# Optimization experiments

Measured on AMD Instinct MI355X. Metric: run time of the kernel, lower is better.

## Reference

```python
import jax, jax.numpy as jnp
import numpy as np

PRED_LEN = 256
K = 32
LOW_FREQ = 1


def setup_inputs() -> dict:
    key = jax.random.key(0)
    x = jax.random.normal(key, (8, 1024, 512), dtype=jnp.float32)
    return {"x": x}


def _fourier_layer(x):
    b, t, d = x.shape
    # per-channel standardization over time (torch .std is unbiased -> ddof=1)
    x_mean = jnp.mean(x, axis=1, keepdims=True)                      # (b,1,d)
    x_std = jnp.std(x, axis=1, keepdims=True, ddof=1) + 1e-8         # (b,1,d)
    xs = jnp.clip((x - x_mean) / x_std, -2.0, 2.0) + 1e-9

    # rfft over time; t is even and LOW_FREQ < t//2 -> drop DC..low_freq-1 and Nyquist
    x_freq = jnp.fft.rfft(xs, axis=1)[:, LOW_FREQ:-1]                # (b,N,d) complex64
    n_freq = x_freq.shape[1]
    f = jnp.fft.rfftfreq(t).astype(jnp.float32)[LOW_FREQ:n_freq + LOW_FREQ]  # (N,)

    # top-k frequencies by amplitude, independently per (batch, channel)
    amp_all = jnp.abs(x_freq).astype(jnp.float32)                    # (b,N,d)
    _, idx = jax.lax.top_k(jnp.transpose(amp_all, (0, 2, 1)), K)     # (b,d,k)
    idx = jnp.transpose(idx, (0, 2, 1))                              # (b,k,d)
    xf = jnp.take_along_axis(x_freq, idx, axis=1)                    # (b,k,d)
    f_sel = f[idx]                                                   # (b,k,d)

    # extrapolate: conjugate pair -> real signal, sum of k cosines
    xf2 = jnp.concatenate([xf, jnp.conj(xf)], axis=1)                # (b,2k,d)
    f2 = jnp.concatenate([f_sel, -f_sel], axis=1)[:, :, None, :]     # (b,2k,1,d)
    T = t + PRED_LEN
    t_val = jnp.arange(T, dtype=jnp.float32)[None, None, :, None]    # (1,1,T,1)
    amp = (jnp.abs(xf2) / (t + 1e-8))[:, :, None, :]                 # (b,2k,1,d)
    phase = jnp.clip(jnp.angle(xf2), -np.pi, np.pi)[:, :, None, :]   # (b,2k,1,d)
    angle = 2.0 * np.pi * f2 * t_val + phase                         # (b,2k,T,d)
    angle = angle - 2.0 * np.pi * jnp.floor(angle / (2.0 * np.pi))
    x_time = jnp.sum(amp * jnp.cos(angle), axis=1)                   # (b,T,d)

    return x_time * x_std + x_mean


def reference(x):
    return _fourier_layer(x)
```

## Files before the change

kernel.cpp:

```cpp
#include <hip/hip_runtime.h>

#define T_IN 1024
#define D_DIM 512
#define T_OUT 1280
#define NPAIR 4096

__global__ __launch_bounds__(256) void transpose_kernel(const float* __restrict__ x,
                                                        float* __restrict__ xt,
                                                        double2* __restrict__ tw) {
    __shared__ float tile[64][65];
    const int b  = blockIdx.z;
    const int t0 = blockIdx.y * 64;
    const int d0 = blockIdx.x * 64;
    const int dl = threadIdx.x & 63;
    const int r0 = threadIdx.x >> 6;

    if (blockIdx.x < 4 && blockIdx.y == 0 && blockIdx.z == 0) {
        int m = blockIdx.x * 256 + threadIdx.x;
        double th = (6.283185307179586476925286766559 / 1024.0) * (double)m;
        tw[m] = make_double2(cos(th), -sin(th));
    }

#pragma unroll
    for (int i = 0; i < 16; ++i) {
        int tl = r0 * 16 + i;
        tile[tl][dl] = x[((size_t)b * T_IN + (t0 + tl)) * D_DIM + d0 + dl];
    }
    __syncthreads();
#pragma unroll
    for (int i = 0; i < 16; ++i) {
        int dl2 = r0 * 16 + i;
        xt[((size_t)b * D_DIM + (d0 + dl2)) * T_IN + t0 + dl] = tile[dl][dl2];
    }
}

__device__ __forceinline__ double2 TW8(const double2* __restrict__ E, int m) {
    int r = m & 255;
    int q = (m >> 8) & 3;
    double c, s;
    if (r <= 128) { double2 t = E[r];       c = t.x; s = t.y; }
    else          { double2 t = E[256 - r]; c = t.y; s = t.x; }
    double C, S;
    switch (q) {
        case 0:  C = c;  S = s;  break;
        case 1:  C = -s; S = c;  break;
        case 2:  C = -c; S = -s; break;
        default: C = s;  S = -c; break;
    }
    return make_double2(C, -S);
}

__global__ __launch_bounds__(256) void dft_kernel(const float* __restrict__ xt,
                                                  const double2* __restrict__ twg,
                                                  float2* __restrict__ stats,
                                                  float4* __restrict__ sel) {
    __shared__ double2 uni[1024];
    __shared__ double2 tw_s[130];
    __shared__ double  red_s[16];
    double* xs_s = (double*)uni;

    const int tid  = threadIdx.x;
    const int pair = blockIdx.x;

    const float4 v = reinterpret_cast<const float4*>(xt + (size_t)pair * T_IN)[tid];

    if (tid < 130) {
        double2 t = twg[tid];
        tw_s[tid] = make_double2(t.x, -t.y);
    }

    double sum = (double)v.x + (double)v.y + (double)v.z + (double)v.w;
    double sq  = (double)v.x * v.x + (double)v.y * v.y +
                 (double)v.z * v.z + (double)v.w * v.w;
#pragma unroll
    for (int off = 32; off; off >>= 1) {
        sum += __shfl_down(sum, off);
        sq  += __shfl_down(sq, off);
    }
    const int wv   = tid >> 6;
    const int lane = tid & 63;
    if (lane == 0) { red_s[wv] = sum; red_s[8 + wv] = sq; }
    __syncthreads();
    double mean, stdp;
    {
        double s = red_s[0] + red_s[1] + red_s[2] + red_s[3];
        double q = red_s[8] + red_s[9] + red_s[10] + red_s[11];
        mean = s * (1.0 / 1024.0);
        double var = (q - 1024.0 * mean * mean) * (1.0 / 1023.0);
        var = var > 0.0 ? var : 0.0;
        stdp = sqrt(var) + 1e-8;
        if (tid == 0) stats[pair] = make_float2((float)mean, (float)stdp);
    }
    const double inv = 1.0 / stdp;
    {
        double z0 = ((double)v.x - mean) * inv;
        double z1 = ((double)v.y - mean) * inv;
        double z2 = ((double)v.z - mean) * inv;
        double z3 = ((double)v.w - mean) * inv;
        z0 = fmin(2.0, fmax(-2.0, z0)) + 1e-9;
        z1 = fmin(2.0, fmax(-2.0, z1)) + 1e-9;
        z2 = fmin(2.0, fmax(-2.0, z2)) + 1e-9;
        z3 = fmin(2.0, fmax(-2.0, z3)) + 1e-9;
        xs_s[tid * 4 + 0] = z0;
        xs_s[tid * 4 + 1] = z1;
        xs_s[tid * 4 + 2] = z2;
        xs_s[tid * 4 + 3] = z3;
    }
    __syncthreads();

    {
        int idx = tid;
#pragma unroll
        for (int rr = 0; rr < 2; ++rr) {
            if (idx < 480) {
                int t1p = 1 + (idx >> 5);
                int t2c = idx & 31;
                int ia = t1p * 32 + t2c;
                int ib = (32 - t1p) * 32 + t2c;
                double a = xs_s[ia], b = xs_s[ib];
                xs_s[ia] = a + b;
                xs_s[ib] = a - b;
            }
            idx += 256;
        }
    }
    __syncthreads();

    const int k1 = tid & 31;
    const int g  = tid >> 5;

    double2 R0, R1, R2, R3;
    {
        const double2 w = TW8(tw_s, k1 * 32);
        const double sgn16 = (k1 & 1) ? -1.0 : 1.0;

        double ar0 = xs_s[g]      + sgn16 * xs_s[512 + g];
        double ar1 = xs_s[g + 8]  + sgn16 * xs_s[512 + g + 8];
        double ar2 = xs_s[g + 16] + sgn16 * xs_s[512 + g + 16];
        double ar3 = xs_s[g + 24] + sgn16 * xs_s[512 + g + 24];
        double ai0 = 0, ai1 = 0, ai2 = 0, ai3 = 0;

        double c = w.x, s = w.y;
#pragma unroll 5
        for (int t1 = 1; t1 <= 15; ++t1) {
            const double* eb = &xs_s[t1 * 32];
            const double* ob = &xs_s[(32 - t1) * 32];
            ar0 = fma(eb[g], c, ar0);      ai0 = fma(ob[g], s, ai0);
            ar1 = fma(eb[g + 8], c, ar1);  ai1 = fma(ob[g + 8], s, ai1);
            ar2 = fma(eb[g + 16], c, ar2); ai2 = fma(ob[g + 16], s, ai2);
            ar3 = fma(eb[g + 24], c, ar3); ai3 = fma(ob[g + 24], s, ai3);
            double cn = c * w.x - s * w.y;
            double sn = s * w.x + c * w.y;
            c = cn; s = sn;
        }
        {
            double2 tm = TW8(tw_s, g * k1);
            R0 = make_double2(ar0 * tm.x - ai0 * tm.y, ar0 * tm.y + ai0 * tm.x);
        }
        {
            double2 tm = TW8(tw_s, (g + 8) * k1);
            R1 = make_double2(ar1 * tm.x - ai1 * tm.y, ar1 * tm.y + ai1 * tm.x);
        }
        {
            double2 tm = TW8(tw_s, (g + 16) * k1);
            R2 = make_double2(ar2 * tm.x - ai2 * tm.y, ar2 * tm.y + ai2 * tm.x);
        }
        {
            double2 tm = TW8(tw_s, (g + 24) * k1);
            R3 = make_double2(ar3 * tm.x - ai3 * tm.y, ar3 * tm.y + ai3 * tm.x);
        }
    }
    __syncthreads();

    uni[g * 32 + k1]        = R0;
    uni[(g + 8) * 32 + k1]  = R1;
    uni[(g + 16) * 32 + k1] = R2;
    uni[(g + 24) * 32 + k1] = R3;
    __syncthreads();

    double Ar = 0, Ai = 0, Br = 0, Bi = 0;
    {
        const double2 wa = TW8(tw_s, 32 * g);
        const double sg = (g & 1) ? -1.0 : 1.0;
        double ca = 1.0, sa = 0.0;
#pragma unroll
        for (int u = 0; u < 4; ++u) {
            {
                const int t2 = 4 * u + 0;
                double2 S  = uni[t2 * 32 + k1];
                double2 S2 = uni[(t2 + 16) * 32 + k1];
                double Ex = fma(sg, S2.x, S.x);
                double Ey = fma(sg, S2.y, S.y);
                double P = fma(Ex, ca, -(Ey * sa));
                double Q = fma(Ex, sa,  (Ey * ca));
                Ar += P; Ai += Q; Br += P; Bi += Q;
                double cn = fma(ca, wa.x, -(sa * wa.y));
                double sn = fma(sa, wa.x,  (ca * wa.y));
                ca = cn; sa = sn;
            }
            {
                const int t2 = 4 * u + 1;
                double2 S  = uni[t2 * 32 + k1];
                double2 S2 = uni[(t2 + 16) * 32 + k1];
                double Ex = fma(sg, S2.x, S.x);
                double Ey = fma(sg, S2.y, S.y);
                double P = fma(Ex, ca, -(Ey * sa));
                double Q = fma(Ex, sa,  (Ey * ca));
                Ar += P; Ai += Q; Br += Q; Bi -= P;
                double cn = fma(ca, wa.x, -(sa * wa.y));
                double sn = fma(sa, wa.x,  (ca * wa.y));
                ca = cn; sa = sn;
            }
            {
                const int t2 = 4 * u + 2;
                double2 S  = uni[t2 * 32 + k1];
                double2 S2 = uni[(t2 + 16) * 32 + k1];
                double Ex = fma(sg, S2.x, S.x);
                double Ey = fma(sg, S2.y, S.y);
                double P = fma(Ex, ca, -(Ey * sa));
                double Q = fma(Ex, sa,  (Ey * ca));
                Ar += P; Ai += Q; Br -= P; Bi -= Q;
                double cn = fma(ca, wa.x, -(sa * wa.y));
                double sn = fma(sa, wa.x,  (ca * wa.y));
                ca = cn; sa = sn;
            }
            {
                const int t2 = 4 * u + 3;
                double2 S  = uni[t2 * 32 + k1];
                double2 S2 = uni[(t2 + 16) * 32 + k1];
                double Ex = fma(sg, S2.x, S.x);
                double Ey = fma(sg, S2.y, S.y);
                double P = fma(Ex, ca, -(Ey * sa));
                double Q = fma(Ex, sa,  (Ey * ca));
                Ar += P; Ai += Q; Br -= Q; Bi += P;
                double cn = fma(ca, wa.x, -(sa * wa.y));
                double sn = fma(sa, wa.x,  (ca * wa.y));
                ca = cn; sa = sn;
            }
        }
    }
    const int ka = k1 + 32 * g;
    const int kb = ka + 256;

    unsigned long long uA, uB;
    {
        double a2a = Ar * Ar + Ai * Ai;
        double a2b = Br * Br + Bi * Bi;
        unsigned long long bba = __double_as_longlong(a2a);
        unsigned long long bbb = __double_as_longlong(a2b);
        double keya = __longlong_as_double((bba & ~1023ULL) |
                                           (unsigned long long)(1023 - ka));
        double keyb = __longlong_as_double((bbb & ~1023ULL) |
                                           (unsigned long long)(1023 - kb));
        if (ka == 0) keya = -1.0;
        unsigned long long a = (unsigned long long)__double_as_longlong(keya);
        unsigned long long b = (unsigned long long)__double_as_longlong(keyb);
        uA = a ^ ((a >> 63) ? 0xFFFFFFFFFFFFFFFFULL : 0x8000000000000000ULL);
        uB = b ^ ((b >> 63) ? 0xFFFFFFFFFFFFFFFFULL : 0x8000000000000000ULL);
    }

    __syncthreads();
    float2* spec_f = (float2*)uni;
    double* cand   = (double*)(uni + 512);
    spec_f[ka] = make_float2((float)Ar, (float)Ai);
    spec_f[kb] = make_float2((float)Br, (float)Bi);

    const unsigned long long lt = lane ? (0xFFFFFFFFFFFFFFFFULL >> (64 - lane))
                                       : 0ULL;
    {
        unsigned long long pref = 0;
        for (int bit = 63; bit >= 0; --bit) {
            unsigned long long trial = pref | (1ULL << bit);
            int cnt = __popcll(__ballot(uA >= trial)) +
                      __popcll(__ballot(uB >= trial));
            if (cnt >= 32) pref = trial;
        }
        unsigned long long mA = __ballot(uA >= pref);
        unsigned long long mB = __ballot(uB >= pref);
        const int bs = wv * 32;
        if (uA >= pref)
            cand[bs + __popcll(mA & lt)] =
                __longlong_as_double((long long)uA);
        if (uB >= pref)
            cand[bs + __popcll(mA) + __popcll(mB & lt)] =
                __longlong_as_double((long long)uB);
    }
    __syncthreads();

    if (tid < 64) {
        unsigned long long c0 =
            (unsigned long long)__double_as_longlong(cand[tid]);
        unsigned long long c1 =
            (unsigned long long)__double_as_longlong(cand[tid + 64]);
        unsigned long long pref = 0;
        for (int bit = 63; bit >= 0; --bit) {
            unsigned long long trial = pref | (1ULL << bit);
            int cnt = __popcll(__ballot(c0 >= trial)) +
                      __popcll(__ballot(c1 >= trial));
            if (cnt >= 32) pref = trial;
        }
        unsigned long long m0 = __ballot(c0 >= pref);
        unsigned long long m1 = __ballot(c1 >= pref);
        const float C = 6.28318530717958647692f / 1024.0f;
        const size_t sb = (size_t)pair * 32;
        if (c0 >= pref) {
            int slot = __popcll(m0 & lt);
            int k = 1023 - (int)(c0 & 1023ULL);
            float2 sp = spec_f[k];
            float ph = atan2f(sp.y, sp.x);
            double key = __longlong_as_double(
                (long long)(c0 ^ 0x8000000000000000ULL));
            double amp = sqrt(key);
            float aout = (float)(2.0 * amp / (1024.0 + 1e-8));
            float tkc = __cosf((float)k * C);
            sel[sb + slot] = make_float4(aout, ph, (float)k, tkc);
        }
        if (c1 >= pref) {
            int slot = __popcll(m0) + __popcll(m1 & lt);
            int k = 1023 - (int)(c1 & 1023ULL);
            float2 sp = spec_f[k];
            float ph = atan2f(sp.y, sp.x);
            double key = __longlong_as_double(
                (long long)(c1 ^ 0x8000000000000000ULL));
            double amp = sqrt(key);
            float aout = (float)(2.0 * amp / (1024.0 + 1e-8));
            float tkc = __cosf((float)k * C);
            sel[sb + slot] = make_float4(aout, ph, (float)k, tkc);
        }
    }
}

__global__ __launch_bounds__(256) void recon_kernel(const float4* __restrict__ sel,
                                                    const float2* __restrict__ stats,
                                                    float* __restrict__ out) {
    __shared__ float4 sel_s[32][65];
    __shared__ float2 st_s[64];
    const int bid   = blockIdx.x;
    const int chunk = bid & 15;
    const int dt    = (bid >> 4) & 7;
    const int b     = bid >> 7;
    const int d0    = dt * 64;
    const int tid   = threadIdx.x;
#pragma unroll
    for (int it = 0; it < 8; ++it) {
        int i   = tid + it * 256;
        int j   = i & 31;
        int dls = i >> 5;
        sel_s[j][dls] = sel[((size_t)(b * D_DIM + d0 + dls)) * 32 + j];
    }
    if (tid < 64) st_s[tid] = stats[b * D_DIM + d0 + tid];
    __syncthreads();

    const int dl    = tid & 63;
    const int wvv   = tid >> 6;
    const int tbase = chunk * 64 + wvv * 16;

    float acc[16];
#pragma unroll
    for (int j = 0; j < 16; ++j) acc[j] = 0.0f;

    const float C = 6.28318530717958647692f / 1024.0f;
#pragma unroll 2
    for (int js = 0; js < 32; ++js) {
        float4 tr = sel_s[js][dl];
        const float a = tr.x;
        int k = (int)tr.z;
        float ck = tr.w;
        float sk = sqrtf(fmaxf(1.0f - ck * ck, 0.0f));
        int mm0 = (k * tbase) & 1023;
        float ang0 = fmaf((float)mm0, C, tr.y);
        float s0, c0;
        __sincosf(ang0, &s0, &c0);
        float c1 = c0 * ck - s0 * sk;
        float K2 = ck + ck;
        acc[0] = fmaf(a, c0, acc[0]);
        acc[1] = fmaf(a, c1, acc[1]);
#pragma unroll
        for (int j = 2; j < 16; ++j) {
            float c2 = fmaf(K2, c1, -c0);
            acc[j] = fmaf(a, c2, acc[j]);
            c0 = c1; c1 = c2;
        }
    }
    const float2 st = st_s[dl];
#pragma unroll
    for (int j = 0; j < 16; ++j) {
        float o = fmaf(acc[j], st.y, st.x);
        int t = tbase + j;
        out[((size_t)b * T_OUT + t) * D_DIM + d0 + dl] = o;
        if (t < 256)
            out[((size_t)b * T_OUT + t + 1024) * D_DIM + d0 + dl] = o;
    }
}

extern "C" void kernel_launch(void* const* d_in, const int* in_sizes, int n_in,
                              void* d_out, int out_size, void* d_ws, size_t ws_size,
                              hipStream_t stream) {
    const float* x = (const float*)d_in[0];
    float* out = (float*)d_out;
    char* ws = (char*)d_ws;
    const size_t MB = 1024 * 1024;

    float*   xt    = (float*)ws;
    double2* tw    = (double2*)(ws + 16 * MB);
    float2*  stats = (float2*)(ws + 16 * MB + 65536);
    float4*  sel   = (float4*)(ws + 16 * MB + 131072);

    transpose_kernel<<<dim3(8, 16, 8), 256, 0, stream>>>(x, xt, tw);
    dft_kernel<<<NPAIR, 256, 0, stream>>>(xt, tw, stats, sel);
    recon_kernel<<<1024, 256, 0, stream>>>(sel, stats, out);
}
```

Before: 77.83 us.

## Radix-4 top-k bit search, pre-butterfly FFT stage, octant twiddle table

The twiddle table shrinks to one octant of 65 entries, and the other values are rebuilt with a 1/sqrt(2) rotation. This halves shared-memory loading in exchange for extra ALU work per lookup. The 16-point combine is folded into the store of the first DFT stage, so the second stage reads one value per step instead of two. The 64-step bitwise radix select for the top-32 threshold becomes 32 radix-4 steps, each with three independent ballots. This halves the serial dependency chain at the cost of more ballot instructions.

Measured after the change: 77.94 us. Within noise of the previous version (+0.1%).

```diff
diff --git a/kernel.cpp b/kernel.cpp
--- a/kernel.cpp
+++ b/kernel.cpp
@@ -34,12 +34,22 @@
     }
 }
 
-__device__ __forceinline__ double2 TW8(const double2* __restrict__ E, int m) {
+__device__ __forceinline__ double2 TW16(const double2* __restrict__ E, int m) {
+    const double RS2 = 0.70710678118654752440084436210485;
     int r = m & 255;
     int q = (m >> 8) & 3;
+    int r2 = (r <= 128) ? r : 256 - r;
+    double cc, ss;
+    if (r2 <= 64) {
+        double2 t = E[r2];
+        cc = t.x; ss = t.y;
+    } else {
+        double2 t = E[128 - r2];
+        cc = (t.x + t.y) * RS2;
+        ss = (t.x - t.y) * RS2;
+    }
     double c, s;
-    if (r <= 128) { double2 t = E[r];       c = t.x; s = t.y; }
-    else          { double2 t = E[256 - r]; c = t.y; s = t.x; }
+    if (r > 128) { c = ss; s = cc; } else { c = cc; s = ss; }
     double C, S;
     switch (q) {
         case 0:  C = c;  S = s;  break;
@@ -55,7 +65,7 @@
                                                   float2* __restrict__ stats,
                                                   float4* __restrict__ sel) {
     __shared__ double2 uni[1024];
-    __shared__ double2 tw_s[130];
+    __shared__ double2 tw_s[65];
     __shared__ double  red_s[16];
     double* xs_s = (double*)uni;
 
@@ -64,7 +74,7 @@
 
     const float4 v = reinterpret_cast<const float4*>(xt + (size_t)pair * T_IN)[tid];
 
-    if (tid < 130) {
+    if (tid < 65) {
         double2 t = twg[tid];
         tw_s[tid] = make_double2(t.x, -t.y);
     }
@@ -131,7 +141,7 @@
 
     double2 R0, R1, R2, R3;
     {
-        const double2 w = TW8(tw_s, k1 * 32);
+        const double2 w = TW16(tw_s, k1 * 32);
         const double sgn16 = (k1 & 1) ? -1.0 : 1.0;
 
         double ar0 = xs_s[g]      + sgn16 * xs_s[512 + g];
@@ -154,84 +164,68 @@
             c = cn; s = sn;
         }
         {
-            double2 tm = TW8(tw_s, g * k1);
+            double2 tm = TW16(tw_s, g * k1);
             R0 = make_double2(ar0 * tm.x - ai0 * tm.y, ar0 * tm.y + ai0 * tm.x);
         }
         {
-            double2 tm = TW8(tw_s, (g + 8) * k1);
+            double2 tm = TW16(tw_s, (g + 8) * k1);
             R1 = make_double2(ar1 * tm.x - ai1 * tm.y, ar1 * tm.y + ai1 * tm.x);
         }
         {
-            double2 tm = TW8(tw_s, (g + 16) * k1);
+            double2 tm = TW16(tw_s, (g + 16) * k1);
             R2 = make_double2(ar2 * tm.x - ai2 * tm.y, ar2 * tm.y + ai2 * tm.x);
         }
         {
-            double2 tm = TW8(tw_s, (g + 24) * k1);
+            double2 tm = TW16(tw_s, (g + 24) * k1);
             R3 = make_double2(ar3 * tm.x - ai3 * tm.y, ar3 * tm.y + ai3 * tm.x);
         }
     }
     __syncthreads();
 
-    uni[g * 32 + k1]        = R0;
-    uni[(g + 8) * 32 + k1]  = R1;
-    uni[(g + 16) * 32 + k1] = R2;
-    uni[(g + 24) * 32 + k1] = R3;
+    uni[g * 32 + k1]        = make_double2(R0.x + R2.x, R0.y + R2.y);
+    uni[(g + 16) * 32 + k1] = make_double2(R0.x - R2.x, R0.y - R2.y);
+    uni[(g + 8) * 32 + k1]  = make_double2(R1.x + R3.x, R1.y + R3.y);
+    uni[(g + 24) * 32 + k1] = make_double2(R1.x - R3.x, R1.y - R3.y);
     __syncthreads();
 
     double Ar = 0, Ai = 0, Br = 0, Bi = 0;
     {
-        const double2 wa = TW8(tw_s, 32 * g);
-        const double sg = (g & 1) ? -1.0 : 1.0;
+        const double2 wa = TW16(tw_s, 32 * g);
+        const int ebase = (g & 1) ? 16 * 32 : 0;
         double ca = 1.0, sa = 0.0;
 #pragma unroll
         for (int u = 0; u < 4; ++u) {
             {
-                const int t2 = 4 * u + 0;
-                double2 S  = uni[t2 * 32 + k1];
-                double2 S2 = uni[(t2 + 16) * 32 + k1];
-                double Ex = fma(sg, S2.x, S.x);
-                double Ey = fma(sg, S2.y, S.y);
-                double P = fma(Ex, ca, -(Ey * sa));
-                double Q = fma(Ex, sa,  (Ey * ca));
+                double2 E = uni[ebase + (4 * u + 0) * 32 + k1];
+                double P = fma(E.x, ca, -(E.y * sa));
+                double Q = fma(E.x, sa,  (E.y * ca));
                 Ar += P; Ai += Q; Br += P; Bi += Q;
                 double cn = fma(ca, wa.x, -(sa * wa.y));
                 double sn = fma(sa, wa.x,  (ca * wa.y));
                 ca = cn; sa = sn;
             }
             {
-                const int t2 = 4 * u + 1;
-                double2 S  = uni[t2 * 32 + k1];
-                double2 S2 = uni[(t2 + 16) * 32 + k1];
-                double Ex = fma(sg, S2.x, S.x);
-                double Ey = fma(sg, S2.y, S.y);
-                double P = fma(Ex, ca, -(Ey * sa));
-                double Q = fma(Ex, sa,  (Ey * ca));
+                double2 E = uni[ebase + (4 * u + 1) * 32 + k1];
+                double P = fma(E.x, ca, -(E.y * sa));
+                double Q = fma(E.x, sa,  (E.y * ca));
                 Ar += P; Ai += Q; Br += Q; Bi -= P;
                 double cn = fma(ca, wa.x, -(sa * wa.y));
                 double sn = fma(sa, wa.x,  (ca * wa.y));
                 ca = cn; sa = sn;
             }
             {
-                const int t2 = 4 * u + 2;
-                double2 S  = uni[t2 * 32 + k1];
-                double2 S2 = uni[(t2 + 16) * 32 + k1];
-                double Ex = fma(sg, S2.x, S.x);
-                double Ey = fma(sg, S2.y, S.y);
-                double P = fma(Ex, ca, -(Ey * sa));
-                double Q = fma(Ex, sa,  (Ey * ca));
+                double2 E = uni[ebase + (4 * u + 2) * 32 + k1];
+                double P = fma(E.x, ca, -(E.y * sa));
+                double Q = fma(E.x, sa,  (E.y * ca));
                 Ar += P; Ai += Q; Br -= P; Bi -= Q;
                 double cn = fma(ca, wa.x, -(sa * wa.y));
                 double sn = fma(sa, wa.x,  (ca * wa.y));
                 ca = cn; sa = sn;
             }
             {
-                const int t2 = 4 * u + 3;
-                double2 S  = uni[t2 * 32 + k1];
-                double2 S2 = uni[(t2 + 16) * 32 + k1];
-                double Ex = fma(sg, S2.x, S.x);
-                double Ey = fma(sg, S2.y, S.y);
-                double P = fma(Ex, ca, -(Ey * sa));
-                double Q = fma(Ex, sa,  (Ey * ca));
+                double2 E = uni[ebase + (4 * u + 3) * 32 + k1];
+                double P = fma(E.x, ca, -(E.y * sa));
+                double Q = fma(E.x, sa,  (E.y * ca));
                 Ar += P; Ai += Q; Br -= Q; Bi += P;
                 double cn = fma(ca, wa.x, -(sa * wa.y));
                 double sn = fma(sa, wa.x,  (ca * wa.y));
@@ -269,11 +263,18 @@
                                        : 0ULL;
     {
         unsigned long long pref = 0;
-        for (int bit = 63; bit >= 0; --bit) {
-            unsigned long long trial = pref | (1ULL << bit);
-            int cnt = __popcll(__ballot(uA >= trial)) +
-                      __popcll(__ballot(uB >= trial));
-            if (cnt >= 32) pref = trial;
+#pragma unroll 4
+        for (int step = 0; step < 32; ++step) {
+            const int sh = 62 - 2 * step;
+            unsigned long long T1 = pref | (1ULL << sh);
+            unsigned long long T2 = pref | (2ULL << sh);
+            unsigned long long T3 = pref | (3ULL << sh);
+            int n3 = __popcll(__ballot(uA >= T3)) + __popcll(__ballot(uB >= T3));
+            int n2 = __popcll(__ballot(uA >= T2)) + __popcll(__ballot(uB >= T2));
+            int n1 = __popcll(__ballot(uA >= T1)) + __popcll(__ballot(uB >= T1));
+            if (n3 >= 32)      pref = T3;
+            else if (n2 >= 32) pref = T2;
+            else if (n1 >= 32) pref = T1;
         }
         unsigned long long mA = __ballot(uA >= pref);
         unsigned long long mB = __ballot(uB >= pref);
@@ -293,11 +294,18 @@
         unsigned long long c1 =
             (unsigned long long)__double_as_longlong(cand[tid + 64]);
         unsigned long long pref = 0;
-        for (int bit = 63; bit >= 0; --bit) {
-            unsigned long long trial = pref | (1ULL << bit);
-            int cnt = __popcll(__ballot(c0 >= trial)) +
-                      __popcll(__ballot(c1 >= trial));
-            if (cnt >= 32) pref = trial;
+#pragma unroll 4
+        for (int step = 0; step < 32; ++step) {
+            const int sh = 62 - 2 * step;
+            unsigned long long T1 = pref | (1ULL << sh);
+            unsigned long long T2 = pref | (2ULL << sh);
+            unsigned long long T3 = pref | (3ULL << sh);
+            int n3 = __popcll(__ballot(c0 >= T3)) + __popcll(__ballot(c1 >= T3));
+            int n2 = __popcll(__ballot(c0 >= T2)) + __popcll(__ballot(c1 >= T2));
+            int n1 = __popcll(__ballot(c0 >= T1)) + __popcll(__ballot(c1 >= T1));
+            if (n3 >= 32)      pref = T3;
+            else if (n2 >= 32) pref = T2;
+            else if (n1 >= 32) pref = T1;
         }
         unsigned long long m0 = __ballot(c0 >= pref);
         unsigned long long m1 = __ballot(c1 >= pref);
```
